# Kernel optimization log

Hardware: AMD Instinct MI355X
Metric: run time of the kernel (lower is better)

Reference implementation:

```python
import jax, jax.numpy as jnp
import numpy as np

ALPHA = 0.2          # LeakyReLU negative slope
NEG_INF = -9e15      # mask value used by the original module


def setup_inputs() -> dict:
    key = jax.random.key(0)
    k1, k2, k3, k4 = jax.random.split(key, 4)
    N, Din, Dout = 8192, 512, 256
    features = jax.random.normal(k1, (N, Din), dtype=jnp.float32)
    adj = jax.random.randint(k2, (N, N), 0, 2, dtype=jnp.int32)
    W = jax.random.normal(k3, (Din, Dout), dtype=jnp.float32) * (1.414 / np.sqrt(Din))
    a = jax.random.normal(k4, (2 * Dout, 1), dtype=jnp.float32) * (1.414 / np.sqrt(2 * Dout))
    return {"features": features, "adj": adj, "W": W, "a": a}


def reference(features, adj, W, a):
    Dout = W.shape[1]
    Wh = features @ W                       # [N, Dout]
    # e_ij = leakyrelu([Wh_i || Wh_j] @ a) decomposes additively:
    # identical math to the N*N*2D concat in the original, without materializing it.
    src = Wh @ a[:Dout, 0]                  # [N]  contribution of node i
    dst = Wh @ a[Dout:, 0]                  # [N]  contribution of node j
    e = jax.nn.leaky_relu(src[:, None] + dst[None, :], negative_slope=ALPHA)  # [N, N]
    masked = jnp.where(adj > 0, e, NEG_INF)
    attention = jax.nn.softmax(masked, axis=1)   # dropout p=0.0 (eval) -> identity
    h_prime = attention @ Wh                # [N, Dout]
    return jax.nn.elu(h_prime)
```

## Files before the change

### kernel.cpp

```cpp
#include <hip/hip_runtime.h>
#include <hip/hip_bf16.h>

#define NN   8192
#define DIN  512
#define DOUT 256

typedef __attribute__((ext_vector_type(8)))  short s16x8;
typedef __attribute__((ext_vector_type(16))) float f32x16;

static __device__ __forceinline__ unsigned short f2bf(float f) {
    union { float f; unsigned u; } v; v.f = f;
    unsigned r = v.u + 0x7fffu + ((v.u >> 16) & 1u);
    return (unsigned short)(r >> 16);
}

static __device__ __forceinline__ void gload_lds16(const void* g, void* l) {
    __builtin_amdgcn_global_load_lds(
        (const __attribute__((address_space(1))) unsigned int*)g,
        (__attribute__((address_space(3))) unsigned int*)l, 16, 0, 0);
}

__global__ __launch_bounds__(256) void k_wh2(const float* __restrict__ feat,
                                             const float* __restrict__ W,
                                             const float* __restrict__ a,
                                             unsigned short* __restrict__ WhT,
                                             float* __restrict__ src,
                                             float* __restrict__ dst) {
    __shared__ float lf[16 * DIN];
    __shared__ float red[2][4][16];
    const int tid = threadIdx.x;
    const int i0  = blockIdx.x * 16;
    const int w   = tid >> 6, lane = tid & 63;

    const float4* fsrc = (const float4*)(feat + (size_t)i0 * DIN);
    float4* fdst = (float4*)lf;
    #pragma unroll
    for (int q = 0; q < 8; ++q) fdst[tid + q * 256] = fsrc[tid + q * 256];
    __syncthreads();

    const int c = tid;
    float outs[16];
    #pragma unroll
    for (int r = 0; r < 16; ++r) outs[r] = 0.f;

    for (int k = 0; k < DIN; k += 4) {
        float w0 = W[(k + 0) * DOUT + c];
        float w1 = W[(k + 1) * DOUT + c];
        float w2 = W[(k + 2) * DOUT + c];
        float w3 = W[(k + 3) * DOUT + c];
        #pragma unroll
        for (int r = 0; r < 16; ++r) {
            float4 f = *(const float4*)&lf[r * DIN + k];
            outs[r] = fmaf(f.x, w0, fmaf(f.y, w1, fmaf(f.z, w2, fmaf(f.w, w3, outs[r]))));
        }
    }

    unsigned short tb[16];
    #pragma unroll
    for (int r = 0; r < 16; ++r) tb[r] = f2bf(outs[r]);
    uint4* wt = (uint4*)(WhT + (size_t)c * NN + i0);
    wt[0] = *(uint4*)&tb[0];
    wt[1] = *(uint4*)&tb[8];

    const float as_ = a[c], ad_ = a[DOUT + c];
    #pragma unroll
    for (int r = 0; r < 16; ++r) {
        float s = outs[r] * as_;
        float d = outs[r] * ad_;
        #pragma unroll
        for (int off = 32; off; off >>= 1) {
            s += __shfl_xor(s, off);
            d += __shfl_xor(d, off);
        }
        if (lane == 0) { red[0][w][r] = s; red[1][w][r] = d; }
    }
    __syncthreads();
    if (tid < 16)
        src[i0 + tid] = red[0][0][tid] + red[0][1][tid] + red[0][2][tid] + red[0][3][tid];
    else if (tid < 32) {
        int r = tid - 16;
        dst[i0 + r] = red[1][0][r] + red[1][1][r] + red[1][2][r] + red[1][3][r];
    }
}

__global__ __launch_bounds__(512, 4) void k_attn3(const int* __restrict__ adj,
                                                  const unsigned short* __restrict__ WhT,
                                                  const float* __restrict__ src,
                                                  const float* __restrict__ dstg,
                                                  float* __restrict__ denp,
                                                  float* __restrict__ part) {
    __shared__ __attribute__((aligned(16))) char Bs[2][32768];
    __shared__ __attribute__((aligned(16))) char Pl[8192];

    const int tid  = threadIdx.x;
    const int lane = tid & 63;
    const int w    = tid >> 6;
    const int l31  = lane & 31, lhi = lane >> 5;
    const int c0w  = w * 32;

    const int rt  = blockIdx.x & 127;
    const int ks  = blockIdx.x >> 7;
    const int kb0 = ks * 2048;

    const int r  = tid >> 3, kb = tid & 7;
    const int gr = rt * 64 + r;
    const float si = src[gr];
    const int*   adjR = adj  + (size_t)gr * NN + kb0 + kb * 8;
    const float* dstp = dstg +                   kb0 + kb * 8;
    const int pbyte = r * 128 + ((kb * 16) ^ ((r & 7) << 4));

    int colB[4], kbB[4];
    #pragma unroll
    for (int q = 0; q < 4; ++q) {
        int chunk = q * 512 + tid;
        colB[q] = chunk >> 3;
        kbB[q]  = ((chunk & 7) * 16) ^ ((colB[q] & 7) << 4);
    }

    f32x16 acc[2];
    #pragma unroll
    for (int mt = 0; mt < 2; ++mt)
        #pragma unroll
        for (int e = 0; e < 16; ++e) acc[mt][e] = 0.f;
    float den = 0.f;

    #pragma unroll
    for (int q = 0; q < 4; ++q)
        gload_lds16((const char*)WhT + (size_t)colB[q] * (NN * 2) + (size_t)kb0 * 2 + kbB[q],
                    (char*)Bs[0] + (q * 512 + tid) * 16);
    int4 a0 = *(const int4*)(adjR);
    int4 a1 = *(const int4*)(adjR + 4);
    __syncthreads();

    for (int t = 0; t < 32; ++t) {
        const int cur = t & 1;
        int4 na0, na1;
        if (t < 31) {
            na0 = *(const int4*)(adjR + (t + 1) * 64);
            na1 = *(const int4*)(adjR + (t + 1) * 64 + 4);
            const size_t gkb = (size_t)(kb0 + (t + 1) * 64) * 2;
            #pragma unroll
            for (int q = 0; q < 4; ++q)
                gload_lds16((const char*)WhT + (size_t)colB[q] * (NN * 2) + gkb + kbB[q],
                            (char*)Bs[cur ^ 1] + (q * 512 + tid) * 16);
        }
        float4 d0 = *(const float4*)(dstp + t * 64);
        float4 d1 = *(const float4*)(dstp + t * 64 + 4);
        const float dd[8] = {d0.x, d0.y, d0.z, d0.w, d1.x, d1.y, d1.z, d1.w};
        const int   va[8] = {a0.x, a0.y, a0.z, a0.w, a1.x, a1.y, a1.z, a1.w};
        s16x8 pw;
        #pragma unroll
        for (int jj = 0; jj < 8; ++jj) {
            float x = si + dd[jj];
            x = fmaxf(x, 0.2f * x);
            float p = va[jj] > 0 ? __expf(x) : 0.f;
            den += p;
            pw[jj] = (short)f2bf(p);
        }
        *(s16x8*)(Pl + pbyte) = pw;
        a0 = na0; a1 = na1;
        __syncthreads();

        #pragma unroll
        for (int ks4 = 0; ks4 < 4; ++ks4) {
            const int kbyte = ks4 * 32 + lhi * 16;
            const int colg  = c0w + l31;
            s16x8 bf = *(const s16x8*)(Bs[cur] + colg * 128 + (kbyte ^ ((colg & 7) << 4)));
            #pragma unroll
            for (int mt = 0; mt < 2; ++mt) {
                const int row = mt * 32 + l31;
                s16x8 af = *(const s16x8*)(Pl + row * 128 + (kbyte ^ ((row & 7) << 4)));
                acc[mt] = __builtin_amdgcn_mfma_f32_32x32x16_bf16(af, bf, acc[mt], 0, 0, 0);
            }
        }
        __syncthreads();
    }

    den += __shfl_xor(den, 1);
    den += __shfl_xor(den, 2);
    den += __shfl_xor(den, 4);
    if ((tid & 7) == 0) denp[(size_t)ks * NN + gr] = den;

    float* pp = part + (size_t)ks * (NN * DOUT);
    #pragma unroll
    for (int mt = 0; mt < 2; ++mt) {
        #pragma unroll
        for (int e = 0; e < 16; ++e) {
            const int row = rt * 64 + mt * 32 + (e & 3) + 8 * (e >> 2) + 4 * lhi;
            pp[(size_t)row * DOUT + c0w + l31] = acc[mt][e];
        }
    }
}

__global__ __launch_bounds__(256) void k_finish2(const float* __restrict__ part,
                                                 const float* __restrict__ denp,
                                                 float* __restrict__ out) {
    const int idx = blockIdx.x * 256 + threadIdx.x;
    const int row = idx >> 6;
    float den = denp[row] + denp[NN + row] + denp[2 * NN + row] + denp[3 * NN + row];
    float rv = den > 0.f ? 1.f / den : 0.f;
    const int st = NN * DOUT / 4;
    const float4* p = (const float4*)part;
    float4 va = p[idx], vb = p[idx + st], vc = p[idx + 2 * st], vd = p[idx + 3 * st];
    float4 s;
    s.x = (va.x + vb.x + vc.x + vd.x) * rv;
    s.y = (va.y + vb.y + vc.y + vd.y) * rv;
    s.z = (va.z + vb.z + vc.z + vd.z) * rv;
    s.w = (va.w + vb.w + vc.w + vd.w) * rv;
    s.x = s.x > 0.f ? s.x : expm1f(s.x);
    s.y = s.y > 0.f ? s.y : expm1f(s.y);
    s.z = s.z > 0.f ? s.z : expm1f(s.z);
    s.w = s.w > 0.f ? s.w : expm1f(s.w);
    ((float4*)out)[idx] = s;
}

extern "C" void kernel_launch(void* const* d_in, const int* in_sizes, int n_in,
                              void* d_out, int out_size, void* d_ws, size_t ws_size,
                              hipStream_t stream) {
    const float* feat = (const float*)d_in[0];
    const int*   adj  = (const int*)d_in[1];
    const float* W    = (const float*)d_in[2];
    const float* a    = (const float*)d_in[3];
    float* out = (float*)d_out;

    char* ws = (char*)d_ws;
    unsigned short* WhT  = (unsigned short*)ws;
    float*          src  = (float*)(ws + 4194304);
    float*          dst  = (float*)(ws + 4227072);
    float*          denp = (float*)(ws + 4259840);
    float*          part = (float*)(ws + 4390912);

    k_wh2    <<<512,  256, 0, stream>>>(feat, W, a, WhT, src, dst);
    k_attn3  <<<512,  512, 0, stream>>>(adj, WhT, src, dst, denp, part);
    k_finish2<<<2048, 256, 0, stream>>>(part, denp, out);
}
```

Before: 185.9 us.

## Double-buffer P tile and use one barrier per step in attention loop

The attention kernel now keeps two LDS buffers for the probability tile. The main loop is unrolled by two with a macro and uses a single s_barrier per step instead of two __syncthreads. An explicit s_waitcnt and sched_barrier control when the WhT prefetch for the next step is issued: after the barrier, overlapping the MFMA work. This aims to cut barrier stalls and expose more overlap between global-to-LDS loads and matrix math, at the cost of more LDS and a redundant final prefetch. The hand-written waitcnt could become fragile if the compiler reorders memory operations.

After: 180.3 us. 1.03x faster.

```diff
diff --git a/kernel.cpp b/kernel.cpp
--- a/kernel.cpp
+++ b/kernel.cpp
@@ -83,14 +83,68 @@
     }
 }
 
-__global__ __launch_bounds__(512, 4) void k_attn3(const int* __restrict__ adj,
+
+#define STEP_BODY(T, CUR, A0, A1, NA0, NA1)                                              \
+{                                                                                        \
+                       \
+    {                                                                                    \
+        const int tn_ = ((T) < 31) ? (T) + 1 : 31;        \
+        NA0 = *(const int4*)(adjR + tn_ * 64);                                           \
+        NA1 = *(const int4*)(adjR + tn_ * 64 + 4);                                       \
+    }                                                                                    \
+    {                                                                                    \
+        float4 d0_ = *(const float4*)(dstp + (T) * 64);                                  \
+        float4 d1_ = *(const float4*)(dstp + (T) * 64 + 4);                              \
+        const float dd_[8] = {d0_.x, d0_.y, d0_.z, d0_.w, d1_.x, d1_.y, d1_.z, d1_.w};   \
+        const int   va_[8] = {A0.x, A0.y, A0.z, A0.w, A1.x, A1.y, A1.z, A1.w};           \
+        s16x8 pw_;                                                                       \
+        _Pragma("unroll")                                                                \
+        for (int jj = 0; jj < 8; ++jj) {                                                 \
+            float x_ = si + dd_[jj];                                                     \
+            x_ = fmaxf(x_, 0.2f * x_);                               \
+            float p_ = va_[jj] > 0 ? __expf(x_) : 0.f;  \
+            den += p_;                                                                   \
+            pw_[jj] = (short)f2bf(p_);                                                   \
+        }                                                                                \
+        *(s16x8*)(Pl[CUR] + pbyte) = pw_;                                                \
+    }                                                                                    \
+    __builtin_amdgcn_sched_barrier(0);                                                   \
+    asm volatile("s_waitcnt vmcnt(2) lgkmcnt(0)" ::: "memory");                          \
+    __builtin_amdgcn_s_barrier();                                                        \
+    __builtin_amdgcn_sched_barrier(0);                                                   \
+            \
+    {                                                                                    \
+        const int tn_ = ((T) < 31) ? (T) + 1 : 31;                                       \
+        const size_t gkb_ = (size_t)(kb0 + tn_ * 64) * 2;                                \
+        _Pragma("unroll")                                                                \
+        for (int q = 0; q < 4; ++q)                                                      \
+            gload_lds16((const char*)WhT + (size_t)colB[q] * (NN * 2) + gkb_ + kbB[q],   \
+                        Bs[(CUR) ^ 1] + (q * 512 + tid) * 16);                           \
+    }                                                                                    \
+    _Pragma("unroll")                                                                    \
+    for (int ks4 = 0; ks4 < 4; ++ks4) {                                                  \
+        const int kbyte_ = ks4 * 32 + lhi * 16;                                          \
+        const int colg_  = c0w + l31;                                                    \
+        s16x8 bfv_ = *(const s16x8*)(Bs[CUR] + colg_ * 128 +                             \
+                                     (kbyte_ ^ ((colg_ & 7) << 4)));                     \
+        _Pragma("unroll")                                                                \
+        for (int mt = 0; mt < 2; ++mt) {                                                 \
+            const int row_ = mt * 32 + l31;                                              \
+            s16x8 afv_ = *(const s16x8*)(Pl[CUR] + row_ * 128 +                          \
+                                         (kbyte_ ^ ((row_ & 7) << 4)));                  \
+            acc[mt] = __builtin_amdgcn_mfma_f32_32x32x16_bf16(afv_, bfv_, acc[mt], 0, 0, 0); \
+        }                                                                                \
+    }                                                                                    \
+}
+
+__global__ __launch_bounds__(512, 4) void k_attn4(const int* __restrict__ adj,
                                                   const unsigned short* __restrict__ WhT,
                                                   const float* __restrict__ src,
                                                   const float* __restrict__ dstg,
                                                   float* __restrict__ denp,
                                                   float* __restrict__ part) {
     __shared__ __attribute__((aligned(16))) char Bs[2][32768];
-    __shared__ __attribute__((aligned(16))) char Pl[8192];
+    __shared__ __attribute__((aligned(16))) char Pl[2][8192];
 
     const int tid  = threadIdx.x;
     const int lane = tid & 63;
@@ -127,53 +181,14 @@
     #pragma unroll
     for (int q = 0; q < 4; ++q)
         gload_lds16((const char*)WhT + (size_t)colB[q] * (NN * 2) + (size_t)kb0 * 2 + kbB[q],
-                    (char*)Bs[0] + (q * 512 + tid) * 16);
+                    Bs[0] + (q * 512 + tid) * 16);
     int4 a0 = *(const int4*)(adjR);
     int4 a1 = *(const int4*)(adjR + 4);
-    __syncthreads();
-
-    for (int t = 0; t < 32; ++t) {
-        const int cur = t & 1;
-        int4 na0, na1;
-        if (t < 31) {
-            na0 = *(const int4*)(adjR + (t + 1) * 64);
-            na1 = *(const int4*)(adjR + (t + 1) * 64 + 4);
-            const size_t gkb = (size_t)(kb0 + (t + 1) * 64) * 2;
-            #pragma unroll
-            for (int q = 0; q < 4; ++q)
-                gload_lds16((const char*)WhT + (size_t)colB[q] * (NN * 2) + gkb + kbB[q],
-                            (char*)Bs[cur ^ 1] + (q * 512 + tid) * 16);
-        }
-        float4 d0 = *(const float4*)(dstp + t * 64);
-        float4 d1 = *(const float4*)(dstp + t * 64 + 4);
-        const float dd[8] = {d0.x, d0.y, d0.z, d0.w, d1.x, d1.y, d1.z, d1.w};
-        const int   va[8] = {a0.x, a0.y, a0.z, a0.w, a1.x, a1.y, a1.z, a1.w};
-        s16x8 pw;
-        #pragma unroll
-        for (int jj = 0; jj < 8; ++jj) {
-            float x = si + dd[jj];
-            x = fmaxf(x, 0.2f * x);
-            float p = va[jj] > 0 ? __expf(x) : 0.f;
-            den += p;
-            pw[jj] = (short)f2bf(p);
-        }
-        *(s16x8*)(Pl + pbyte) = pw;
-        a0 = na0; a1 = na1;
-        __syncthreads();
-
-        #pragma unroll
-        for (int ks4 = 0; ks4 < 4; ++ks4) {
-            const int kbyte = ks4 * 32 + lhi * 16;
-            const int colg  = c0w + l31;
-            s16x8 bf = *(const s16x8*)(Bs[cur] + colg * 128 + (kbyte ^ ((colg & 7) << 4)));
-            #pragma unroll
-            for (int mt = 0; mt < 2; ++mt) {
-                const int row = mt * 32 + l31;
-                s16x8 af = *(const s16x8*)(Pl + row * 128 + (kbyte ^ ((row & 7) << 4)));
-                acc[mt] = __builtin_amdgcn_mfma_f32_32x32x16_bf16(af, bf, acc[mt], 0, 0, 0);
-            }
-        }
-        __syncthreads();
+    int4 n0, n1;
+
+    for (int tt = 0; tt < 16; ++tt) {
+        STEP_BODY(2 * tt,     0, a0, a1, n0, n1);
+        STEP_BODY(2 * tt + 1, 1, n0, n1, a0, a1);
     }
 
     den += __shfl_xor(den, 1);
@@ -231,6 +246,6 @@
     float*          part = (float*)(ws + 4390912);
 
     k_wh2    <<<512,  256, 0, stream>>>(feat, W, a, WhT, src, dst);
-    k_attn3  <<<512,  512, 0, stream>>>(adj, WhT, src, dst, denp, part);
+    k_attn4  <<<512,  512, 0, stream>>>(adj, WhT, src, dst, denp, part);
     k_finish2<<<2048, 256, 0, stream>>>(part, denp, out);
 }
```

## Pack adjacency into bitmask and split attention columns across XCD-mapped blocks

Applied to the files above, without the earlier changes.

A new pre-pass compresses the int32 adjacency matrix into a 1-bit-per-edge mask, so the attention kernel reads 32x fewer mask bytes. Each block now covers only half of the output columns with 256 threads, and its split-K and column indices are derived from the block id modulo 8 to match the XCD layout. The probability tile for the next step is computed after the MFMA loop and between explicit barriers, with raised wave priority during the MFMAs. The cost is an extra full pass over adj, and each mask/exp tile is now computed twice, once per column half.

New measurement: 206.3 us. +11.0%, slower.

```diff
diff --git a/kernel.cpp b/kernel.cpp
--- a/kernel.cpp
+++ b/kernel.cpp
@@ -83,13 +83,29 @@
     }
 }
 
-__global__ __launch_bounds__(512, 4) void k_attn3(const int* __restrict__ adj,
+__global__ __launch_bounds__(256) void k_mask(const int* __restrict__ adj,
+                                              unsigned char* __restrict__ bits) {
+    const int row = blockIdx.x;
+    const int tid = threadIdx.x;
+    const int* base = adj + (size_t)row * NN + tid * 32;
+    unsigned int u = 0;
+    #pragma unroll
+    for (int j = 0; j < 8; ++j) {
+        int4 v = *(const int4*)(base + j * 4);
+        unsigned int b = (v.x > 0 ? 1u : 0u) | (v.y > 0 ? 2u : 0u) |
+                         (v.z > 0 ? 4u : 0u) | (v.w > 0 ? 8u : 0u);
+        u |= b << (j * 4);
+    }
+    *(unsigned int*)(bits + (size_t)row * 1024 + tid * 4) = u;
+}
+
+__global__ __launch_bounds__(256, 4) void k_attn8(const unsigned char* __restrict__ bits,
                                                   const unsigned short* __restrict__ WhT,
                                                   const float* __restrict__ src,
                                                   const float* __restrict__ dstg,
                                                   float* __restrict__ denp,
                                                   float* __restrict__ part) {
-    __shared__ __attribute__((aligned(16))) char Bs[2][32768];
+    __shared__ __attribute__((aligned(16))) char Bs[2][16384];
     __shared__ __attribute__((aligned(16))) char Pl[8192];
 
     const int tid  = threadIdx.x;
@@ -98,23 +114,29 @@
     const int l31  = lane & 31, lhi = lane >> 5;
     const int c0w  = w * 32;
 
-    const int rt  = blockIdx.x & 127;
-    const int ks  = blockIdx.x >> 7;
-    const int kb0 = ks * 2048;
-
-    const int r  = tid >> 3, kb = tid & 7;
+    const int bid  = blockIdx.x;
+    const int xcd  = bid & 7;
+    const int ks   = xcd >> 1;
+    const int cs   = xcd & 1;
+    const int rt   = bid >> 3;
+    const int kb0  = ks * 2048;
+    const int cbase = cs * 128;
+
+    const int r  = tid >> 2, kb = tid & 3;
     const int gr = rt * 64 + r;
     const float si = src[gr];
-    const int*   adjR = adj  + (size_t)gr * NN + kb0 + kb * 8;
-    const float* dstp = dstg +                   kb0 + kb * 8;
-    const int pbyte = r * 128 + ((kb * 16) ^ ((r & 7) << 4));
-
-    int colB[4], kbB[4];
+    const unsigned char* browp = bits + (size_t)gr * 1024 + ks * 256 + kb * 2;
+    const float* dstp = dstg + kb0 + kb * 16;
+    const int pb0 = r * 128 + (((kb * 32)      ) ^ ((r & 7) << 4));
+    const int pb1 = r * 128 + (((kb * 32) + 16 ) ^ ((r & 7) << 4));
+
+    const char* gsrcB[4];
     #pragma unroll
     for (int q = 0; q < 4; ++q) {
-        int chunk = q * 512 + tid;
-        colB[q] = chunk >> 3;
-        kbB[q]  = ((chunk & 7) * 16) ^ ((colB[q] & 7) << 4);
+        int chunk = q * 256 + tid;
+        int col   = chunk >> 3;
+        int kbB   = ((chunk & 7) * 16) ^ ((col & 7) << 4);
+        gsrcB[q]  = (const char*)WhT + ((size_t)(cbase + col) * NN + kb0) * 2 + kbB;
     }
 
     f32x16 acc[2];
@@ -126,60 +148,89 @@
 
     #pragma unroll
     for (int q = 0; q < 4; ++q)
-        gload_lds16((const char*)WhT + (size_t)colB[q] * (NN * 2) + (size_t)kb0 * 2 + kbB[q],
-                    (char*)Bs[0] + (q * 512 + tid) * 16);
-    int4 a0 = *(const int4*)(adjR);
-    int4 a1 = *(const int4*)(adjR + 4);
-    __syncthreads();
+        gload_lds16(gsrcB[q], Bs[0] + (q * 256 + tid) * 16);
+    {
+        const unsigned int m16 = *(const unsigned short*)(browp);
+        float4 pd[4];
+        #pragma unroll
+        for (int h = 0; h < 4; ++h) pd[h] = ((const float4*)(dstp))[h];
+        const float* pdf = (const float*)pd;
+        s16x8 pw0, pw1;
+        #pragma unroll
+        for (int jj = 0; jj < 8; ++jj) {
+            float x0 = si + pdf[jj];
+            x0 = fmaxf(x0, 0.2f * x0);
+            float p0 = (m16 >> jj) & 1u ? __expf(x0) : 0.f;
+            float x1 = si + pdf[8 + jj];
+            x1 = fmaxf(x1, 0.2f * x1);
+            float p1 = (m16 >> (8 + jj)) & 1u ? __expf(x1) : 0.f;
+            den += p0 + p1;
+            pw0[jj] = (short)f2bf(p0);
+            pw1[jj] = (short)f2bf(p1);
+        }
+        *(s16x8*)(Pl + pb0) = pw0;
+        *(s16x8*)(Pl + pb1) = pw1;
+    }
+    asm volatile("s_waitcnt vmcnt(0) lgkmcnt(0)" ::: "memory");
+    __builtin_amdgcn_s_barrier();
 
     for (int t = 0; t < 32; ++t) {
         const int cur = t & 1;
-        int4 na0, na1;
         if (t < 31) {
-            na0 = *(const int4*)(adjR + (t + 1) * 64);
-            na1 = *(const int4*)(adjR + (t + 1) * 64 + 4);
-            const size_t gkb = (size_t)(kb0 + (t + 1) * 64) * 2;
             #pragma unroll
             for (int q = 0; q < 4; ++q)
-                gload_lds16((const char*)WhT + (size_t)colB[q] * (NN * 2) + gkb + kbB[q],
-                            (char*)Bs[cur ^ 1] + (q * 512 + tid) * 16);
-        }
-        float4 d0 = *(const float4*)(dstp + t * 64);
-        float4 d1 = *(const float4*)(dstp + t * 64 + 4);
-        const float dd[8] = {d0.x, d0.y, d0.z, d0.w, d1.x, d1.y, d1.z, d1.w};
-        const int   va[8] = {a0.x, a0.y, a0.z, a0.w, a1.x, a1.y, a1.z, a1.w};
-        s16x8 pw;
-        #pragma unroll
-        for (int jj = 0; jj < 8; ++jj) {
-            float x = si + dd[jj];
-            x = fmaxf(x, 0.2f * x);
-            float p = va[jj] > 0 ? __expf(x) : 0.f;
-            den += p;
-            pw[jj] = (short)f2bf(p);
-        }
-        *(s16x8*)(Pl + pbyte) = pw;
-        a0 = na0; a1 = na1;
-        __syncthreads();
-
+                gload_lds16(gsrcB[q] + (size_t)(t + 1) * 128,
+                            Bs[cur ^ 1] + (q * 256 + tid) * 16);
+        }
+        unsigned int m16 = 0;
+        float4 pd[4];
+        if (t < 31) {
+            m16 = *(const unsigned short*)(browp + (t + 1) * 8);
+            #pragma unroll
+            for (int h = 0; h < 4; ++h) pd[h] = ((const float4*)(dstp + (t + 1) * 64))[h];
+        }
+        __builtin_amdgcn_s_setprio(1);
         #pragma unroll
         for (int ks4 = 0; ks4 < 4; ++ks4) {
             const int kbyte = ks4 * 32 + lhi * 16;
-            const int colg  = c0w + l31;
-            s16x8 bf = *(const s16x8*)(Bs[cur] + colg * 128 + (kbyte ^ ((colg & 7) << 4)));
+            const int colL  = c0w + l31;
+            s16x8 bfv = *(const s16x8*)(Bs[cur] + colL * 128 + (kbyte ^ ((colL & 7) << 4)));
             #pragma unroll
             for (int mt = 0; mt < 2; ++mt) {
-                const int row = mt * 32 + l31;
-                s16x8 af = *(const s16x8*)(Pl + row * 128 + (kbyte ^ ((row & 7) << 4)));
-                acc[mt] = __builtin_amdgcn_mfma_f32_32x32x16_bf16(af, bf, acc[mt], 0, 0, 0);
+                const int rowL = mt * 32 + l31;
+                s16x8 afv = *(const s16x8*)(Pl + rowL * 128 + (kbyte ^ ((rowL & 7) << 4)));
+                acc[mt] = __builtin_amdgcn_mfma_f32_32x32x16_bf16(afv, bfv, acc[mt], 0, 0, 0);
             }
         }
-        __syncthreads();
+        __builtin_amdgcn_s_setprio(0);
+        __builtin_amdgcn_sched_barrier(0);
+        __builtin_amdgcn_s_barrier();
+        __builtin_amdgcn_sched_barrier(0);
+        if (t < 31) {
+            const float* pdf = (const float*)pd;
+            s16x8 pw0, pw1;
+            #pragma unroll
+            for (int jj = 0; jj < 8; ++jj) {
+                float x0 = si + pdf[jj];
+                x0 = fmaxf(x0, 0.2f * x0);
+                float p0 = (m16 >> jj) & 1u ? __expf(x0) : 0.f;
+                float x1 = si + pdf[8 + jj];
+                x1 = fmaxf(x1, 0.2f * x1);
+                float p1 = (m16 >> (8 + jj)) & 1u ? __expf(x1) : 0.f;
+                den += p0 + p1;
+                pw0[jj] = (short)f2bf(p0);
+                pw1[jj] = (short)f2bf(p1);
+            }
+            *(s16x8*)(Pl + pb0) = pw0;
+            *(s16x8*)(Pl + pb1) = pw1;
+        }
+        asm volatile("s_waitcnt vmcnt(0) lgkmcnt(0)" ::: "memory");
+        __builtin_amdgcn_s_barrier();
     }
 
     den += __shfl_xor(den, 1);
     den += __shfl_xor(den, 2);
-    den += __shfl_xor(den, 4);
-    if ((tid & 7) == 0) denp[(size_t)ks * NN + gr] = den;
+    if (cs == 0 && (tid & 3) == 0) denp[(size_t)ks * NN + gr] = den;
 
     float* pp = part + (size_t)ks * (NN * DOUT);
     #pragma unroll
@@ -187,7 +238,7 @@
         #pragma unroll
         for (int e = 0; e < 16; ++e) {
             const int row = rt * 64 + mt * 32 + (e & 3) + 8 * (e >> 2) + 4 * lhi;
-            pp[(size_t)row * DOUT + c0w + l31] = acc[mt][e];
+            pp[(size_t)row * DOUT + cbase + c0w + l31] = acc[mt][e];
         }
     }
 }
@@ -228,9 +279,11 @@
     float*          src  = (float*)(ws + 4194304);
     float*          dst  = (float*)(ws + 4227072);
     float*          denp = (float*)(ws + 4259840);
-    float*          part = (float*)(ws + 4390912);
-
+    unsigned char*  bits = (unsigned char*)(ws + 4390912);
+    float*          part = (float*)(ws + 12779520);
+
+    k_mask   <<<8192, 256, 0, stream>>>(adj, bits);
     k_wh2    <<<512,  256, 0, stream>>>(feat, W, a, WhT, src, dst);
-    k_attn3  <<<512,  512, 0, stream>>>(adj, WhT, src, dst, denp, part);
+    k_attn8  <<<1024, 256, 0, stream>>>(bits, WhT, src, dst, denp, part);
     k_finish2<<<2048, 256, 0, stream>>>(part, denp, out);
 }
```
